# Kernel tuning notes

Measured on AMD Instinct MI355X. Metric: run time of the kernel, lower is better.

## Reference

```python
import jax, jax.numpy as jnp
import numpy as np

B, S, DIM = 8, 1024, 192
D2 = 2 * DIM            # inner width 384
CH = 4                  # cell heads (= qk_size)
HD = D2 // CH           # 96 head dim
NB = D2 // 4            # 96 block-diagonal blocks
BLK = D2 // NB          # block size 4
TAU = float(HD) ** 0.5


def setup_inputs() -> dict:
    key = jax.random.key(0)
    ks = jax.random.split(key, 16)
    r = lambda i, shp, s=0.02: jax.random.normal(ks[i], shp, jnp.float32) * s
    return {
        "x": jax.random.normal(ks[0], (B, S, DIM), jnp.float32),
        "ln_g": jnp.ones((DIM,), jnp.float32), "ln_b": jnp.zeros((DIM,), jnp.float32),
        "w1": r(1, (D2, DIM)), "b1": jnp.zeros((D2,), jnp.float32),
        "w2": r(2, (D2, DIM)), "b2": jnp.zeros((D2,), jnp.float32),
        "conv_w": r(3, (D2, 1, 3), 0.1), "conv_b": jnp.zeros((D2,), jnp.float32),
        "qw": r(4, (NB, BLK, BLK), 0.1), "qb": jnp.zeros((D2,), jnp.float32),
        "kw": r(5, (NB, BLK, BLK), 0.1), "kb": jnp.zeros((D2,), jnp.float32),
        "vw": r(6, (NB, BLK, BLK), 0.1), "vb": jnp.zeros((D2,), jnp.float32),
        "wi": r(7, (CH, 3 * D2)), "bi": jax.random.normal(ks[8], (CH,), jnp.float32) * 0.1,
        "wf": r(9, (CH, 3 * D2)), "bf": jnp.linspace(3.0, 6.0, CH).astype(jnp.float32),
        "gn_g": jnp.ones((D2,), jnp.float32), "gn_b": jnp.zeros((D2,), jnp.float32),
        "wo": r(10, (DIM, D2)), "bo": jnp.zeros((DIM,), jnp.float32),
        "skip": jnp.ones((D2,), jnp.float32),
    }


def _layernorm(x, g, b):
    m = x.mean(-1, keepdims=True)
    v = ((x - m) ** 2).mean(-1, keepdims=True)
    return (x - m) / jnp.sqrt(v + 1e-5) * g + b


def _blockdiag(x, w, b):
    # x: [B,S,D2] -> blocks [B,S,NB,BLK]; w: [NB, out_blk, in_blk]
    bs, sq, _ = x.shape
    y = jnp.einsum('bsni,noi->bsno', x.reshape(bs, sq, NB, BLK), w)
    return y.reshape(bs, sq, D2) + b


def _dwconv(x, w, b):
    # depthwise conv over sequence: x [B,S,C] -> [B,C,S] conv -> [B,S,C]
    y = jax.lax.conv_general_dilated(
        x.transpose(0, 2, 1), w, window_strides=(1,), padding=[(1, 1)],
        dimension_numbers=('NCH', 'OIH', 'NCH'), feature_group_count=D2)
    return y.transpose(0, 2, 1) + b


def _cell(q, k, v, wi, bi, wf, bf, gn_g, gn_b):
    bs, sq, _ = q.shape
    gi = jnp.concatenate([q, k, v], axis=-1)                      # [B,S,3*D2]
    it = jnp.einsum('bsc,hc->bhs', gi, wi) + bi[None, :, None]    # [B,H,S]
    ft = jnp.einsum('bsc,hc->bhs', gi, wf) + bf[None, :, None]
    c = jnp.cumsum(jax.nn.log_sigmoid(ft), axis=-1)               # [B,H,S]
    logm = c[..., :, None] - c[..., None, :]                      # cum[i]-cum[j]
    mask = jnp.tril(jnp.ones((sq, sq), dtype=bool))
    f_act = jnp.where(mask, logm, -jnp.inf)
    dt = f_act + it[:, :, None, :]                                # add itilde over cols
    max_d = jnp.max(dt, axis=-1, keepdims=True)
    dmat = jnp.exp(dt - max_d)                                    # [B,H,S,S]
    qh = q.reshape(bs, sq, CH, HD).transpose(0, 2, 1, 3)
    kh = k.reshape(bs, sq, CH, HD).transpose(0, 2, 1, 3)
    vh = v.reshape(bs, sq, CH, HD).transpose(0, 2, 1, 3)
    ct = jnp.einsum('bhid,bhjd->bhij', qh, kh) * dmat / TAU
    maxit = jnp.maximum(jnp.abs(ct.sum(-1, keepdims=True)), jnp.exp(-max_d))
    h = jnp.einsum('bhij,bhjd->bhid', ct, vh) / (maxit + 1e-6)
    h = h.transpose(0, 2, 1, 3).reshape(bs, sq, CH, HD)           # per-token GroupNorm
    mu = h.mean(-1, keepdims=True)
    var = ((h - mu) ** 2).mean(-1, keepdims=True)
    h = (h - mu) / jnp.sqrt(var + 1e-5)
    h = h * gn_g.reshape(CH, HD) + gn_b.reshape(CH, HD)
    return h.reshape(bs, sq, D2)


def reference(x, ln_g, ln_b, w1, b1, w2, b2, conv_w, conv_b, qw, qb, kw, kb,
              vw, vb, wi, bi, wf, bf, gn_g, gn_b, wo, bo, skip):
    inputs = _layernorm(x, ln_g, ln_b)
    a = inputs @ w1.T + b1                   # [B,S,D2]
    bgate = jax.nn.silu(inputs @ w2.T + b2)  # [B,S,D2]
    qk = jax.nn.silu(_dwconv(a, conv_w, conv_b))
    q = _blockdiag(qk, qw, qb)
    k = _blockdiag(qk, kw, kb)
    v = _blockdiag(a, vw, vb)
    out1 = _cell(q, k, v, wi, bi, wf, bf, gn_g, gn_b)
    out1 = (out1 + skip * qk) * bgate
    out = out1 @ wo.T + bo
    return out + x
```

## Files before the change

kernel.cpp:

```cpp
#include <hip/hip_runtime.h>
#include <cstdint>

#define TAU_ 9.797958971132712f

typedef __attribute__((ext_vector_type(4))) float f32x4;
typedef __attribute__((ext_vector_type(8))) short short8;

#define DEV static __device__ __forceinline__

DEV unsigned short f2bf(float f){
  union { float f; unsigned u; } v; v.f = f;
  unsigned r = v.u + 0x7FFFu + ((v.u >> 16) & 1u);
  return (unsigned short)(r >> 16);
}
DEV float bf2f(unsigned short u){
  union { unsigned u; float f; } v; v.u = ((unsigned)u) << 16; return v.f;
}
DEV unsigned pack2bf(float a, float b){
  unsigned r;
  asm("v_cvt_pk_bf16_f32 %0, %1, %2" : "=v"(r) : "v"(a), "v"(b));
  return r;
}
DEV f32x4 ld_bf4(const unsigned short* p){
  uint2 r = *(const uint2*)p;
  f32x4 o;
  o[0] = bf2f((unsigned short)(r.x & 0xffff));
  o[1] = bf2f((unsigned short)(r.x >> 16));
  o[2] = bf2f((unsigned short)(r.y & 0xffff));
  o[3] = bf2f((unsigned short)(r.y >> 16));
  return o;
}
DEV float siluf_(float x){ return x / (1.f + __expf(-x)); }
DEV float logsigf_(float x){ return fminf(x, 0.f) - log1pf(__expf(-fabsf(x))); }

__global__ __launch_bounds__(256) void k1a_ln(
    const float* __restrict__ x, const float* __restrict__ ln_g, const float* __restrict__ ln_b,
    short* __restrict__ xnbf)
{
  const int tid = threadIdx.x;
  const int t = blockIdx.x * 16 + (tid >> 4);
  const int g = tid & 15;
  const float* xr = x + (long)t * 192 + g * 12;
  f32x4 v0 = *(const f32x4*)(xr);
  f32x4 v1 = *(const f32x4*)(xr + 4);
  f32x4 v2 = *(const f32x4*)(xr + 8);
  float s  = v0[0]+v0[1]+v0[2]+v0[3] + v1[0]+v1[1]+v1[2]+v1[3] + v2[0]+v2[1]+v2[2]+v2[3];
  float sq = v0[0]*v0[0]+v0[1]*v0[1]+v0[2]*v0[2]+v0[3]*v0[3]
           + v1[0]*v1[0]+v1[1]*v1[1]+v1[2]*v1[2]+v1[3]*v1[3]
           + v2[0]*v2[0]+v2[1]*v2[1]+v2[2]*v2[2]+v2[3]*v2[3];
  s  += __shfl_xor(s, 1);  s  += __shfl_xor(s, 2);  s  += __shfl_xor(s, 4);  s  += __shfl_xor(s, 8);
  sq += __shfl_xor(sq, 1); sq += __shfl_xor(sq, 2); sq += __shfl_xor(sq, 4); sq += __shfl_xor(sq, 8);
  const float mean = s * (1.f/192.f);
  const float rstd = rsqrtf(sq * (1.f/192.f) - mean * mean + 1e-5f);
  const int c0 = g * 12;
  f32x4 g0 = *(const f32x4*)(ln_g + c0),     b0 = *(const f32x4*)(ln_b + c0);
  f32x4 g1 = *(const f32x4*)(ln_g + c0 + 4), b1 = *(const f32x4*)(ln_b + c0 + 4);
  f32x4 g2 = *(const f32x4*)(ln_g + c0 + 8), b2 = *(const f32x4*)(ln_b + c0 + 8);
  unsigned pk[6];
  pk[0] = pack2bf((v0[0]-mean)*rstd*g0[0]+b0[0], (v0[1]-mean)*rstd*g0[1]+b0[1]);
  pk[1] = pack2bf((v0[2]-mean)*rstd*g0[2]+b0[2], (v0[3]-mean)*rstd*g0[3]+b0[3]);
  pk[2] = pack2bf((v1[0]-mean)*rstd*g1[0]+b1[0], (v1[1]-mean)*rstd*g1[1]+b1[1]);
  pk[3] = pack2bf((v1[2]-mean)*rstd*g1[2]+b1[2], (v1[3]-mean)*rstd*g1[3]+b1[3]);
  pk[4] = pack2bf((v2[0]-mean)*rstd*g2[0]+b2[0], (v2[1]-mean)*rstd*g2[1]+b2[1]);
  pk[5] = pack2bf((v2[2]-mean)*rstd*g2[2]+b2[2], (v2[3]-mean)*rstd*g2[3]+b2[3]);
  uint2* xo = (uint2*)(xnbf + (long)t * 192 + g * 12);
  xo[0] = make_uint2(pk[0], pk[1]);
  xo[1] = make_uint2(pk[2], pk[3]);
  xo[2] = make_uint2(pk[4], pk[5]);
}

__global__ __launch_bounds__(256) void k1b_gemm(
    const short* __restrict__ xnbf,
    const float* __restrict__ w1, const float* __restrict__ w2,
    const float* __restrict__ b1, const float* __restrict__ b2,
    unsigned short* __restrict__ abf, unsigned short* __restrict__ bgate)
{
  __shared__ short wt[18432];
  const int tid = threadIdx.x;
  const int ntg = blockIdx.x & 7;
  const int t0 = (blockIdx.x >> 3) * 64;
  {
    const float* src = (ntg < 4 ? w1 : w2) + (long)(ntg & 3) * 96 * 192;
    #pragma unroll
    for(int i = 0; i < 9; i++){
      const int u = i * 256 + tid;
      const int row = u / 24;
      const int dst = (u * 16) ^ ((row & 7) << 4);
      f32x4 f0 = *(const f32x4*)(src + u * 8);
      f32x4 f1 = *(const f32x4*)(src + u * 8 + 4);
      uint4 pk;
      pk.x = pack2bf(f0[0], f0[1]); pk.y = pack2bf(f0[2], f0[3]);
      pk.z = pack2bf(f1[0], f1[1]); pk.w = pack2bf(f1[2], f1[3]);
      *(uint4*)((char*)wt + dst) = pk;
    }
  }
  __syncthreads();
  const int widx = tid >> 6, lane = tid & 63, qg = lane >> 4, l16 = lane & 15;
  const int mrow = widx * 16 + l16;
  f32x4 acc[6];
  #pragma unroll
  for(int nt = 0; nt < 6; nt++) acc[nt] = (f32x4){0.f,0.f,0.f,0.f};
  const short* xrow = xnbf + (long)(t0 + mrow) * 192;
  #pragma unroll
  for(int kc = 0; kc < 6; kc++){
    short8 af = *(const short8*)(xrow + kc * 32 + 8 * qg);
    #pragma unroll
    for(int nt = 0; nt < 6; nt++){
      const int row = nt * 16 + l16;
      int byte = row * 384 + (kc * 32 + 8 * qg) * 2;
      byte ^= (row & 7) << 4;
      short8 bfr = *(const short8*)((const char*)wt + byte);
      acc[nt] = __builtin_amdgcn_mfma_f32_16x16x32_bf16(af, bfr, acc[nt], 0, 0, 0);
    }
  }
  const int half = ntg >> 2;
  const float* bias = half ? b2 : b1;
  const int ncol = (ntg & 3) * 96;
  #pragma unroll
  for(int nt = 0; nt < 6; nt++){
    const int n = ncol + nt * 16 + l16;
    const float bs = bias[n];
    #pragma unroll
    for(int r = 0; r < 4; r++){
      const int trow = t0 + widx * 16 + 4 * qg + r;
      float v = acc[nt][r] + bs;
      if(half) bgate[(long)trow * 384 + n] = f2bf(siluf_(v));
      else     abf[(long)trow * 384 + n] = f2bf(v);
    }
  }
}

__global__ __launch_bounds__(256) void k2bv(
    const unsigned short* __restrict__ abf,
    const float* __restrict__ cw, const float* __restrict__ cb,
    const float* __restrict__ qw, const float* __restrict__ qb,
    const float* __restrict__ kw, const float* __restrict__ kb,
    const float* __restrict__ vw, const float* __restrict__ vb,
    unsigned short* __restrict__ qkbf, short* __restrict__ qbf, short* __restrict__ kbf,
    short* __restrict__ vtbf)
{
  __shared__ float vt[64][97];
  const int tid = threadIdx.x;
  const int bh = blockIdx.x >> 4;
  const int b = bh >> 2, h = bh & 3;
  const int s0 = (blockIdx.x & 15) << 6;
  #pragma unroll
  for(int it = 0; it < 6; it++){
    const int f = it * 256 + tid;
    const int sl = f / 24, c4l = f % 24;
    const int c4 = h * 24 + c4l;
    const int s = s0 + sl;
    const long t = (long)b * 1024 + s;
    const long abase = t * 384 + c4 * 4;
    f32x4 am = ld_bf4(abf + abase);
    f32x4 al = (s > 0)    ? ld_bf4(abf + abase - 384) : (f32x4){0.f,0.f,0.f,0.f};
    f32x4 ar = (s < 1023) ? ld_bf4(abf + abase + 384) : (f32x4){0.f,0.f,0.f,0.f};
    f32x4 cw0 = *(const f32x4*)(cw + c4 * 12);
    f32x4 cw1 = *(const f32x4*)(cw + c4 * 12 + 4);
    f32x4 cw2 = *(const f32x4*)(cw + c4 * 12 + 8);
    f32x4 cb4 = *(const f32x4*)(cb + c4 * 4);
    f32x4 in;
    in[0] = siluf_(cb4[0] + al[0]*cw0[0] + am[0]*cw0[1] + ar[0]*cw0[2]);
    in[1] = siluf_(cb4[1] + al[1]*cw0[3] + am[1]*cw1[0] + ar[1]*cw1[1]);
    in[2] = siluf_(cb4[2] + al[2]*cw1[2] + am[2]*cw1[3] + ar[2]*cw2[0]);
    in[3] = siluf_(cb4[3] + al[3]*cw2[1] + am[3]*cw2[2] + ar[3]*cw2[3]);
    {
      uint2 pk; pk.x = pack2bf(in[0], in[1]); pk.y = pack2bf(in[2], in[3]);
      *(uint2*)(qkbf + abase) = pk;
    }
    const long base = ((long)(b * 4 + h) * 1024 + s) * 96 + c4l * 4;
    {
      const float* w = qw + c4 * 16;
      float v0 = qb[c4*4+0] + w[0]*in[0]  + w[1]*in[1]  + w[2]*in[2]  + w[3]*in[3];
      float v1 = qb[c4*4+1] + w[4]*in[0]  + w[5]*in[1]  + w[6]*in[2]  + w[7]*in[3];
      float v2 = qb[c4*4+2] + w[8]*in[0]  + w[9]*in[1]  + w[10]*in[2] + w[11]*in[3];
      float v3 = qb[c4*4+3] + w[12]*in[0] + w[13]*in[1] + w[14]*in[2] + w[15]*in[3];
      uint2 pk; pk.x = pack2bf(v0, v1); pk.y = pack2bf(v2, v3);
      *(uint2*)(qbf + base) = pk;
    }
    {
      const float* w = kw + c4 * 16;
      float v0 = kb[c4*4+0] + w[0]*in[0]  + w[1]*in[1]  + w[2]*in[2]  + w[3]*in[3];
      float v1 = kb[c4*4+1] + w[4]*in[0]  + w[5]*in[1]  + w[6]*in[2]  + w[7]*in[3];
      float v2 = kb[c4*4+2] + w[8]*in[0]  + w[9]*in[1]  + w[10]*in[2] + w[11]*in[3];
      float v3 = kb[c4*4+3] + w[12]*in[0] + w[13]*in[1] + w[14]*in[2] + w[15]*in[3];
      uint2 pk; pk.x = pack2bf(v0, v1); pk.y = pack2bf(v2, v3);
      *(uint2*)(kbf + base) = pk;
    }
    {
      const float* w = vw + c4 * 16;
      #pragma unroll
      for(int o = 0; o < 4; o++){
        float v = vb[c4*4+o] + w[o*4]*am[0] + w[o*4+1]*am[1] + w[o*4+2]*am[2] + w[o*4+3]*am[3];
        vt[sl][c4l * 4 + o] = v;
      }
    }
  }
  __syncthreads();
  #pragma unroll
  for(int it = 0; it < 24; it++){
    const int f = it * 256 + tid;
    const int d = f >> 6, sl = f & 63;
    vtbf[((long)bh * 96 + d) * 1024 + s0 + sl] = (short)f2bf(vt[sl][d]);
  }
}

__global__ __launch_bounds__(256) void k2c_gates(
    const short* __restrict__ qbf, const short* __restrict__ kbf,
    const unsigned short* __restrict__ abf,
    const float* __restrict__ vw, const float* __restrict__ vb,
    const float* __restrict__ wi, const float* __restrict__ bi,
    const float* __restrict__ wf, const float* __restrict__ bff,
    float* __restrict__ itv, float* __restrict__ ftv)
{
  const int tid = threadIdx.x;
  const int lane = tid & 63, widx = tid >> 6;
  const int t = blockIdx.x * 4 + widx;
  const int b = t >> 10, s = t & 1023;
  float pit[4] = {0,0,0,0}, pft[4] = {0,0,0,0};
  for(int j = 0; j < 18; j++){
    const int e = lane + 64 * j;
    float val;
    if(e < 768){
      const int c = (e >= 384) ? e - 384 : e;
      const short* src = (e >= 384) ? kbf : qbf;
      const int h = c / 96, d = c - h * 96;
      val = bf2f((unsigned short)src[((long)(b * 4 + h) * 1024 + s) * 96 + d]);
    } else {
      const int c = e - 768;
      const int c4 = c >> 2, o = c & 3;
      f32x4 in = ld_bf4(abf + (long)t * 384 + c4 * 4);
      const float* w = vw + c4 * 16 + o * 4;
      val = vb[c] + w[0]*in[0] + w[1]*in[1] + w[2]*in[2] + w[3]*in[3];
    }
    #pragma unroll
    for(int h = 0; h < 4; h++){
      pit[h] += val * wi[h * 1152 + e];
      pft[h] += val * wf[h * 1152 + e];
    }
  }
  #pragma unroll
  for(int h = 0; h < 4; h++){
    float vi = pit[h], vf = pft[h];
    #pragma unroll
    for(int m = 1; m < 64; m <<= 1){ vi += __shfl_xor(vi, m); vf += __shfl_xor(vf, m); }
    if(lane == 0){
      itv[((long)(b * 4 + h)) * 1024 + s] = vi + bi[h];
      ftv[((long)(b * 4 + h)) * 1024 + s] = vf + bff[h];
    }
  }
}

__global__ __launch_bounds__(256) void k3_scan(
    const float* __restrict__ itv, const float* __restrict__ ftv,
    float* __restrict__ Ev, float* __restrict__ Rpv, float* __restrict__ dsv)
{
  __shared__ float sb[256];
  const int bh = blockIdx.x, tid = threadIdx.x;
  const long base = (long)bh * 1024 + tid * 4;
  f32x4 f4 = *(const f32x4*)(ftv + base);
  const float l0 = logsigf_(f4[0]);
  const float l1 = logsigf_(f4[1]);
  const float l2 = logsigf_(f4[2]);
  const float l3 = logsigf_(f4[3]);
  float c0 = l0, c1 = l0 + l1, c2 = c1 + l2, c3 = c2 + l3;
  sb[tid] = c3;
  __syncthreads();
  for(int off = 1; off < 256; off <<= 1){
    float mine = sb[tid];
    float oth = (tid >= off) ? sb[tid - off] : 0.f;
    __syncthreads();
    sb[tid] = mine + oth;
    __syncthreads();
  }
  const float excl = (tid > 0) ? sb[tid - 1] : 0.f;
  c0 += excl; c1 += excl; c2 += excl; c3 += excl;
  f32x4 i4 = *(const f32x4*)(itv + base);
  const float m0 = i4[0] - c0, m1 = i4[1] - c1, m2 = i4[2] - c2, m3 = i4[3] - c3;
  const float x1 = fmaxf(m0, m1), x2 = fmaxf(x1, m2), x3 = fmaxf(x2, m3);
  __syncthreads();
  sb[tid] = x3;
  __syncthreads();
  for(int off = 1; off < 256; off <<= 1){
    float mine = sb[tid];
    float oth = (tid >= off) ? sb[tid - off] : -3.4e38f;
    __syncthreads();
    sb[tid] = fmaxf(mine, oth);
    __syncthreads();
  }
  const float exm = (tid > 0) ? sb[tid - 1] : -3.4e38f;
  const float M0 = fmaxf(m0, exm);
  const float M1 = fmaxf(x1, exm);
  const float M2 = fmaxf(x2, exm);
  const float M3 = fmaxf(x3, exm);
  f32x4 e, rp, ds;
  e[0] = __expf(m0); e[1] = __expf(m1); e[2] = __expf(m2); e[3] = __expf(m3);
  rp[0] = __expf(-M0) * (1.f/TAU_); rp[1] = __expf(-M1) * (1.f/TAU_);
  rp[2] = __expf(-M2) * (1.f/TAU_); rp[3] = __expf(-M3) * (1.f/TAU_);
  ds[0] = __expf(-(c0 + M0)); ds[1] = __expf(-(c1 + M1));
  ds[2] = __expf(-(c2 + M2)); ds[3] = __expf(-(c3 + M3));
  *(f32x4*)(Ev  + base) = e;
  *(f32x4*)(Rpv + base) = rp;
  *(f32x4*)(dsv + base) = ds;
}

__global__ __launch_bounds__(256, 2) void k4_attn(
    const short* __restrict__ qbf, const short* __restrict__ kbf, const short* __restrict__ vtbf,
    const float* __restrict__ Ev, const float* __restrict__ Rpv, const float* __restrict__ dsv,
    const float* __restrict__ gn_g, const float* __restrict__ gn_b,
    const unsigned short* __restrict__ qkbf, const unsigned short* __restrict__ bgate,
    const float* __restrict__ skip, short* __restrict__ o1bf)
{
  __shared__ short kbuf[2][64 * 104];
  __shared__ short vbuf[2][96 * 72];
  __shared__ float ebuf[2][64];
  __shared__ short P[4][16][72];
  const int tid = threadIdx.x;
  const int w = tid >> 6, lane = tid & 63, qg = lane >> 4, l16 = lane & 15;
  const int xcd = blockIdx.x & 7, q = blockIdx.x >> 3;
  const int bh = ((q & 3) << 3) | xcd;
  const int qh = q >> 2;
  const int ib = (q < 32) ? (15 - qh) : (qh - 8);
  const int i0w = ib * 64 + w * 16;
  const long qkbase = (long)bh * 1024;
  const int nj = ib + 1;

  short8 qf[3];
  #pragma unroll
  for(int kc = 0; kc < 3; kc++)
    qf[kc] = *(const short8*)(qbf + (qkbase + i0w + l16) * 96 + kc * 32 + 8 * qg);
  const float rp = Rpv[qkbase + i0w + l16];
  const float ds = dsv[qkbase + i0w + l16];

  f32x4 acc[6];
  #pragma unroll
  for(int dt = 0; dt < 6; dt++) acc[dt] = (f32x4){0.f,0.f,0.f,0.f};
  float bp = 0.f;

  const int rK0 = tid / 12,        cK0 = tid % 12;
  const int rK1 = (tid+256) / 12,  cK1 = (tid+256) % 12;
  const int rK2 = (tid+512) / 12,  cK2 = (tid+512) % 12;
  const int dV0 = tid >> 3,        cV0 = tid & 7;
  const int dV1 = (tid+256) >> 3,  cV1 = (tid+256) & 7;
  const int dV2 = (tid+512) >> 3,  cV2 = (tid+512) & 7;
  const bool he = (tid < 16);
  short8 sk0, sk1, sk2, sv0, sv1, sv2; f32x4 se;
  const short* kgb = kbf + qkbase * 96;
  const short* vgb = vtbf + (long)bh * 96 * 1024;

#define STAGE_LOAD(J0)                                              \
  {                                                                 \
    const int j0_ = (J0);                                           \
    sk0 = *(const short8*)(kgb + (j0_ + rK0) * 96 + cK0 * 8);       \
    sk1 = *(const short8*)(kgb + (j0_ + rK1) * 96 + cK1 * 8);       \
    sk2 = *(const short8*)(kgb + (j0_ + rK2) * 96 + cK2 * 8);       \
    sv0 = *(const short8*)(vgb + (long)dV0 * 1024 + j0_ + cV0 * 8); \
    sv1 = *(const short8*)(vgb + (long)dV1 * 1024 + j0_ + cV1 * 8); \
    sv2 = *(const short8*)(vgb + (long)dV2 * 1024 + j0_ + cV2 * 8); \
    if(he) se = *(const f32x4*)(Ev + qkbase + j0_ + tid * 4);       \
  }

#define STAGE_WRITE(B)                                   \
  {                                                      \
    *(short8*)(&kbuf[B][rK0 * 104 + cK0 * 8]) = sk0;     \
    *(short8*)(&kbuf[B][rK1 * 104 + cK1 * 8]) = sk1;     \
    *(short8*)(&kbuf[B][rK2 * 104 + cK2 * 8]) = sk2;     \
    *(short8*)(&vbuf[B][dV0 * 72 + cV0 * 8]) = sv0;      \
    *(short8*)(&vbuf[B][dV1 * 72 + cV1 * 8]) = sv1;      \
    *(short8*)(&vbuf[B][dV2 * 72 + cV2 * 8]) = sv2;      \
    if(he) *(f32x4*)(&ebuf[B][tid * 4]) = se;            \
  }

  STAGE_LOAD(0);
  int cur = 0;
  for(int jt = 0; jt < nj; jt++){
    STAGE_WRITE(cur);
    __syncthreads();
    if(jt + 1 < nj) STAGE_LOAD((jt + 1) * 64);

    const int j0 = jt * 64;
    const bool diag = (jt == nj - 1);
    const int i = i0w + l16;
    __builtin_amdgcn_s_setprio(1);
    #pragma unroll
    for(int jsub = 0; jsub < 4; jsub++){
      f32x4 C = (f32x4){0.f,0.f,0.f,0.f};
      #pragma unroll
      for(int kc = 0; kc < 3; kc++){
        short8 kf = *(const short8*)(&kbuf[cur][(jsub*16 + l16) * 104 + kc * 32 + 8 * qg]);
        C = __builtin_amdgcn_mfma_f32_16x16x32_bf16(kf, qf[kc], C, 0, 0, 0);
      }
      f32x4 e4 = *(const f32x4*)(&ebuf[cur][jsub * 16 + 4 * qg]);
      float v0 = C[0] * e4[0];
      float v1 = C[1] * e4[1];
      float v2 = C[2] * e4[2];
      float v3 = C[3] * e4[3];
      if(diag){
        const int jb = j0 + jsub * 16 + 4 * qg;
        if(jb + 0 > i) v0 = 0.f;
        if(jb + 1 > i) v1 = 0.f;
        if(jb + 2 > i) v2 = 0.f;
        if(jb + 3 > i) v3 = 0.f;
      }
      bp += v0 + v1 + v2 + v3;
      uint2 pw; pw.x = pack2bf(v0, v1); pw.y = pack2bf(v2, v3);
      *(uint2*)(&P[w][l16][jsub * 16 + 4 * qg]) = pw;
    }
    asm volatile("s_waitcnt lgkmcnt(0)" ::: "memory");
    #pragma unroll
    for(int ksub = 0; ksub < 2; ksub++){
      short8 pa = *(const short8*)(&P[w][l16][ksub * 32 + 8 * qg]);
      #pragma unroll
      for(int dt = 0; dt < 6; dt++){
        short8 vf = *(const short8*)(&vbuf[cur][(dt * 16 + l16) * 72 + ksub * 32 + 8 * qg]);
        acc[dt] = __builtin_amdgcn_mfma_f32_16x16x32_bf16(pa, vf, acc[dt], 0, 0, 0);
      }
    }
    __builtin_amdgcn_s_setprio(0);
    cur ^= 1;
  }
#undef STAGE_LOAD
#undef STAGE_WRITE

  const int head = bh & 3, bb = bh >> 2;
  float bsum = bp;
  bsum += __shfl_xor(bsum, 16);
  bsum += __shfl_xor(bsum, 32);
  const float bfull = bsum * rp;
  const float den = fmaxf(fabsf(bfull), ds) + 1e-6f;
  const float sc = rp / den;
  float srow[4];
  #pragma unroll
  for(int r = 0; r < 4; r++) srow[r] = __shfl(sc, 4 * qg + r);
  float hv[6][4], mu[4], rs[4];
  #pragma unroll
  for(int r = 0; r < 4; r++){
    float sm = 0.f, sq = 0.f;
    #pragma unroll
    for(int dt = 0; dt < 6; dt++){
      const float h = acc[dt][r] * srow[r];
      hv[dt][r] = h; sm += h; sq += h * h;
    }
    sm += __shfl_xor(sm, 1); sm += __shfl_xor(sm, 2); sm += __shfl_xor(sm, 4); sm += __shfl_xor(sm, 8);
    sq += __shfl_xor(sq, 1); sq += __shfl_xor(sq, 2); sq += __shfl_xor(sq, 4); sq += __shfl_xor(sq, 8);
    const float m_ = sm * (1.f/96.f);
    mu[r] = m_;
    rs[r] = rsqrtf(sq * (1.f/96.f) - m_ * m_ + 1e-5f);
  }
  #pragma unroll
  for(int dt = 0; dt < 6; dt++){
    const int col = head * 96 + dt * 16 + l16;
    const float g  = gn_g[col];
    const float be = gn_b[col];
    const float sk = skip[col];
    #pragma unroll
    for(int r = 0; r < 4; r++){
      const long off = ((long)(bb * 1024 + i0w + 4 * qg + r)) * 384 + col;
      const float hn = (hv[dt][r] - mu[r]) * rs[r] * g + be;
      const float o1 = (hn + sk * bf2f(qkbf[off])) * bf2f(bgate[off]);
      o1bf[off] = (short)f2bf(o1);
    }
  }
}

__global__ __launch_bounds__(256) void k5_gemm(
    const short* __restrict__ o1bf, const float* __restrict__ wo,
    const float* __restrict__ bo, const float* __restrict__ x, float* __restrict__ out)
{
  __shared__ short wt[18432];
  const int tid = threadIdx.x;
  const int ng = blockIdx.x & 3;
  const int t0 = (blockIdx.x >> 2) * 64;
  {
    const float* src = wo + (long)ng * 48 * 384;
    #pragma unroll
    for(int i = 0; i < 9; i++){
      const int u = i * 256 + tid;
      const int row = u / 48;
      const int dst = (u * 16) ^ ((row & 7) << 4);
      f32x4 f0 = *(const f32x4*)(src + u * 8);
      f32x4 f1 = *(const f32x4*)(src + u * 8 + 4);
      uint4 pk;
      pk.x = pack2bf(f0[0], f0[1]); pk.y = pack2bf(f0[2], f0[3]);
      pk.z = pack2bf(f1[0], f1[1]); pk.w = pack2bf(f1[2], f1[3]);
      *(uint4*)((char*)wt + dst) = pk;
    }
  }
  __syncthreads();
  const int widx = tid >> 6, lane = tid & 63, qg = lane >> 4, l16 = lane & 15;
  f32x4 acc[3];
  #pragma unroll
  for(int nt = 0; nt < 3; nt++) acc[nt] = (f32x4){0.f,0.f,0.f,0.f};
  const short* arow = o1bf + (long)(t0 + widx * 16 + l16) * 384;
  #pragma unroll
  for(int kc = 0; kc < 12; kc++){
    short8 af = *(const short8*)(arow + kc * 32 + 8 * qg);
    #pragma unroll
    for(int nt = 0; nt < 3; nt++){
      const int row = nt * 16 + l16;
      int byte = row * 768 + kc * 64 + qg * 16;
      byte ^= (row & 7) << 4;
      short8 bfr = *(const short8*)((const char*)wt + byte);
      acc[nt] = __builtin_amdgcn_mfma_f32_16x16x32_bf16(af, bfr, acc[nt], 0, 0, 0);
    }
  }
  #pragma unroll
  for(int nt = 0; nt < 3; nt++){
    const int n = ng * 48 + nt * 16 + l16;
    const float b_ = bo[n];
    #pragma unroll
    for(int r = 0; r < 4; r++){
      const int trow = t0 + widx * 16 + 4 * qg + r;
      out[(long)trow * 192 + n] = acc[nt][r] + b_ + x[(long)trow * 192 + n];
    }
  }
}

extern "C" void kernel_launch(void* const* d_in, const int* in_sizes, int n_in,
                              void* d_out, int out_size, void* d_ws, size_t ws_size,
                              hipStream_t stream)
{
  (void)in_sizes; (void)n_in; (void)out_size; (void)ws_size;
  const float* x    = (const float*)d_in[0];
  const float* ln_g = (const float*)d_in[1];
  const float* ln_b = (const float*)d_in[2];
  const float* w1   = (const float*)d_in[3];
  const float* b1   = (const float*)d_in[4];
  const float* w2   = (const float*)d_in[5];
  const float* b2   = (const float*)d_in[6];
  const float* cw   = (const float*)d_in[7];
  const float* cb   = (const float*)d_in[8];
  const float* qw   = (const float*)d_in[9];
  const float* qb   = (const float*)d_in[10];
  const float* kw   = (const float*)d_in[11];
  const float* kb   = (const float*)d_in[12];
  const float* vw   = (const float*)d_in[13];
  const float* vb   = (const float*)d_in[14];
  const float* wi   = (const float*)d_in[15];
  const float* bi   = (const float*)d_in[16];
  const float* wf   = (const float*)d_in[17];
  const float* bff  = (const float*)d_in[18];
  const float* gn_g = (const float*)d_in[19];
  const float* gn_b = (const float*)d_in[20];
  const float* wo   = (const float*)d_in[21];
  const float* bo   = (const float*)d_in[22];
  const float* skip = (const float*)d_in[23];
  float* out = (float*)d_out;

  char* ws = (char*)d_ws;
  unsigned short* abf   = (unsigned short*)(ws + 0);
  unsigned short* bgate = (unsigned short*)(ws + 12582912);
  unsigned short* qkbf  = (unsigned short*)(ws + 25165824);
  short* xnbf  = (short*)(ws + 37748736);
  short* o1bf  = (short*)(ws + 41943040);
  short* qbf   = (short*)(ws + 50331648);
  short* kbf   = (short*)(ws + 56623104);
  short* vtbf  = (short*)(ws + 62914560);
  float* itv   = (float*)(ws + 69648384);
  float* ftv   = (float*)(ws + 69779456);
  float* Ev    = (float*)(ws + 69910528);
  float* Rpv   = (float*)(ws + 70041600);
  float* dsv   = (float*)(ws + 70172672);

  k1a_ln<<<512, 256, 0, stream>>>(x, ln_g, ln_b, xnbf);
  k1b_gemm<<<1024, 256, 0, stream>>>(xnbf, w1, w2, b1, b2, abf, bgate);
  k2bv<<<512, 256, 0, stream>>>(abf, cw, cb, qw, qb, kw, kb, vw, vb, qkbf, qbf, kbf, vtbf);
  k2c_gates<<<2048, 256, 0, stream>>>(qbf, kbf, abf, vw, vb, wi, bi, wf, bff, itv, ftv);
  k3_scan<<<32, 256, 0, stream>>>(itv, ftv, Ev, Rpv, dsv);
  k4_attn<<<512, 256, 0, stream>>>(qbf, kbf, vtbf, Ev, Rpv, dsv, gn_g, gn_b,
                                   qkbf, bgate, skip, o1bf);
  k5_gemm<<<512, 256, 0, stream>>>(o1bf, wo, bo, x, out);
}
```

Measured before the change: 88.91 us.

## Move skip/gate epilogue from attention kernel into output GEMM A-load

```diff
diff --git a/kernel.cpp b/kernel.cpp
--- a/kernel.cpp
+++ b/kernel.cpp
@@ -308,8 +308,7 @@
     const short* __restrict__ qbf, const short* __restrict__ kbf, const short* __restrict__ vtbf,
     const float* __restrict__ Ev, const float* __restrict__ Rpv, const float* __restrict__ dsv,
     const float* __restrict__ gn_g, const float* __restrict__ gn_b,
-    const unsigned short* __restrict__ qkbf, const unsigned short* __restrict__ bgate,
-    const float* __restrict__ skip, short* __restrict__ o1bf)
+    short* __restrict__ hnbf)
 {
   __shared__ short kbuf[2][64 * 104];
   __shared__ short vbuf[2][96 * 72];
@@ -447,30 +446,41 @@
     mu[r] = m_;
     rs[r] = rsqrtf(sq * (1.f/96.f) - m_ * m_ + 1e-5f);
   }
+  __syncthreads();
+  short* hstage = &kbuf[0][0];
   #pragma unroll
   for(int dt = 0; dt < 6; dt++){
     const int col = head * 96 + dt * 16 + l16;
     const float g  = gn_g[col];
     const float be = gn_b[col];
-    const float sk = skip[col];
     #pragma unroll
     for(int r = 0; r < 4; r++){
-      const long off = ((long)(bb * 1024 + i0w + 4 * qg + r)) * 384 + col;
       const float hn = (hv[dt][r] - mu[r]) * rs[r] * g + be;
-      const float o1 = (hn + sk * bf2f(qkbf[off])) * bf2f(bgate[off]);
-      o1bf[off] = (short)f2bf(o1);
-    }
+      hstage[(w * 16 + 4 * qg + r) * 104 + dt * 16 + l16] = (short)f2bf(hn);
+    }
+  }
+  __syncthreads();
+  #pragma unroll
+  for(int u2 = 0; u2 < 3; u2++){
+    const int f = u2 * 256 + tid;
+    const int row = f / 12, c8 = f % 12;
+    short8 h8 = *(const short8*)(hstage + row * 104 + c8 * 8);
+    *(short8*)(hnbf + ((long)(bb * 1024 + ib * 64 + row)) * 384 + head * 96 + c8 * 8) = h8;
   }
 }
 
 __global__ __launch_bounds__(256) void k5_gemm(
-    const short* __restrict__ o1bf, const float* __restrict__ wo,
-    const float* __restrict__ bo, const float* __restrict__ x, float* __restrict__ out)
+    const short* __restrict__ hnbf, const unsigned short* __restrict__ qkbf,
+    const unsigned short* __restrict__ bgate, const float* __restrict__ skip,
+    const float* __restrict__ wo, const float* __restrict__ bo,
+    const float* __restrict__ x, float* __restrict__ out)
 {
   __shared__ short wt[18432];
+  __shared__ float sks[384];
   const int tid = threadIdx.x;
   const int ng = blockIdx.x & 3;
   const int t0 = (blockIdx.x >> 2) * 64;
+  if(tid < 96) *(f32x4*)(sks + tid * 4) = *(const f32x4*)(skip + tid * 4);
   {
     const float* src = wo + (long)ng * 48 * 384;
     #pragma unroll
@@ -491,17 +501,28 @@
   f32x4 acc[3];
   #pragma unroll
   for(int nt = 0; nt < 3; nt++) acc[nt] = (f32x4){0.f,0.f,0.f,0.f};
-  const short* arow = o1bf + (long)(t0 + widx * 16 + l16) * 384;
+  const long abase = (long)(t0 + widx * 16 + l16) * 384;
   #pragma unroll
   for(int kc = 0; kc < 12; kc++){
-    short8 af = *(const short8*)(arow + kc * 32 + 8 * qg);
+    const int c0 = kc * 32 + 8 * qg;
+    short8 hf = *(const short8*)(hnbf + abase + c0);
+    short8 q8 = *(const short8*)((const short*)qkbf + abase + c0);
+    short8 g8 = *(const short8*)((const short*)bgate + abase + c0);
+    float o[8];
+    #pragma unroll
+    for(int i = 0; i < 8; i++)
+      o[i] = (bf2f((unsigned short)hf[i]) + sks[c0 + i] * bf2f((unsigned short)q8[i]))
+             * bf2f((unsigned short)g8[i]);
+    union { short8 s; unsigned u4[4]; } af;
+    af.u4[0] = pack2bf(o[0], o[1]); af.u4[1] = pack2bf(o[2], o[3]);
+    af.u4[2] = pack2bf(o[4], o[5]); af.u4[3] = pack2bf(o[6], o[7]);
     #pragma unroll
     for(int nt = 0; nt < 3; nt++){
       const int row = nt * 16 + l16;
       int byte = row * 768 + kc * 64 + qg * 16;
       byte ^= (row & 7) << 4;
       short8 bfr = *(const short8*)((const char*)wt + byte);
-      acc[nt] = __builtin_amdgcn_mfma_f32_16x16x32_bf16(af, bfr, acc[nt], 0, 0, 0);
+      acc[nt] = __builtin_amdgcn_mfma_f32_16x16x32_bf16(af.s, bfr, acc[nt], 0, 0, 0);
     }
   }
   #pragma unroll
@@ -552,7 +573,7 @@
   unsigned short* bgate = (unsigned short*)(ws + 12582912);
   unsigned short* qkbf  = (unsigned short*)(ws + 25165824);
   short* xnbf  = (short*)(ws + 37748736);
-  short* o1bf  = (short*)(ws + 41943040);
+  short* hnbf  = (short*)(ws + 41943040);
   short* qbf   = (short*)(ws + 50331648);
   short* kbf   = (short*)(ws + 56623104);
   short* vtbf  = (short*)(ws + 62914560);
@@ -567,7 +588,6 @@
   k2bv<<<512, 256, 0, stream>>>(abf, cw, cb, qw, qb, kw, kb, vw, vb, qkbf, qbf, kbf, vtbf);
   k2c_gates<<<2048, 256, 0, stream>>>(qbf, kbf, abf, vw, vb, wi, bi, wf, bff, itv, ftv);
   k3_scan<<<32, 256, 0, stream>>>(itv, ftv, Ev, Rpv, dsv);
-  k4_attn<<<512, 256, 0, stream>>>(qbf, kbf, vtbf, Ev, Rpv, dsv, gn_g, gn_b,
-                                   qkbf, bgate, skip, o1bf);
-  k5_gemm<<<512, 256, 0, stream>>>(o1bf, wo, bo, x, out);
-}
+  k4_attn<<<512, 256, 0, stream>>>(qbf, kbf, vtbf, Ev, Rpv, dsv, gn_g, gn_b, hnbf);
+  k5_gemm<<<512, 256, 0, stream>>>(hnbf, qkbf, bgate, skip, wo, bo, x, out);
+}
```

Result: slower. 96.95 us (+9.0%).
